# Performance work log

Measured on AMD Instinct MI355X. Metric: run time of the kernel, lower is better.

The kernel has to match this reference:

```python
import jax, jax.numpy as jnp
import numpy as np

B, D, U = 4096, 1024, 1024

def cumax(a):
    # Faithful to source: softmax over last axis, cumsum over axis 0 (TF defaults).
    return jnp.cumsum(jax.nn.softmax(a, axis=-1), axis=0)

def setup_inputs() -> dict:
    key = jax.random.key(0)
    ks = jax.random.split(key, 21)
    names = ['inputs', 'hidden_prev', 'cell_prev',
             'Wf', 'Uf', 'bf', 'Wi', 'Ui', 'bi', 'Wo', 'Uo', 'bo',
             'Wc', 'Uc', 'bc', 'Wft', 'Uft', 'bft', 'Wit', 'Uit', 'bit']
    shapes = [(B, D), (B, U), (B, U)] + [(D, U), (U, U), (U,)] * 6
    scales = [1.0, 1.0, 1.0] + [0.05, 0.05, 0.05] * 6  # random_normal init ~ small stddev
    return {n: jax.random.normal(k, s, dtype=jnp.float32) * sc
            for n, k, s, sc in zip(names, ks, shapes, scales)}

def reference(inputs, hidden_prev, cell_prev,
              Wf, Uf, bf, Wi, Ui, bi, Wo, Uo, bo,
              Wc, Uc, bc, Wft, Uft, bft, Wit, Uit, bit):
    # Fuse the 12 small GEMMs into 2 big ones: [B,D]@[D,6U] and [B,U]@[U,6U]
    W_all = jnp.concatenate([Wf, Wi, Wo, Wc, Wft, Wit], axis=1)   # [D, 6U]
    U_all = jnp.concatenate([Uf, Ui, Uo, Uc, Uft, Uit], axis=1)   # [U, 6U]
    b_all = jnp.concatenate([bf, bi, bo, bc, bft, bit], axis=0)   # [6U]
    pre = inputs @ W_all + hidden_prev @ U_all + b_all            # [B, 6U]
    zf, zi, zo, zc, zft, zit = [pre[:, j*U:(j+1)*U] for j in range(6)]

    f = jax.nn.sigmoid(zf)
    i = jax.nn.sigmoid(zi)
    o = jax.nn.sigmoid(zo)
    c_hat = jnp.tanh(zc)
    f_tilde = cumax(zft)
    i_tilde = 1.0 - cumax(zit)

    omega = f_tilde * i_tilde
    f_hat = f * omega + (f_tilde - omega)
    i_hat = i * omega + (i_tilde - omega)
    cell = f_hat * cell_prev + i_hat * c_hat
    hidden = o * jnp.tanh(cell)
    return hidden, cell
```

## Files before the change

kernel.cpp:

```cpp
#include <hip/hip_runtime.h>
#include <cstdint>
#include <cstddef>


typedef _Float16 half8  __attribute__((ext_vector_type(8)));
typedef _Float16 half4v __attribute__((ext_vector_type(4)));
typedef float f32x4 __attribute__((ext_vector_type(4)));

__device__ __forceinline__ void async16(const _Float16* g, _Float16* l) {
  __builtin_amdgcn_global_load_lds(
      (const __attribute__((address_space(1))) void*)g,
      (__attribute__((address_space(3))) void*)l, 16, 0, 0);
}

struct Ptrs12 { const float* p[12]; };
struct Ptrs6  { const float* p[6];  };

__global__ void prep(const float* __restrict__ X, const float* __restrict__ H,
                     Ptrs12 w, Ptrs6 bs,
                     _Float16* __restrict__ Ahi, _Float16* __restrict__ Bhi,
                     float* __restrict__ b_all) {
  __shared__ float tile[64][65];
  const int blk = blockIdx.x;
  const int t = threadIdx.x;
  if (blk < 8192) {
    size_t base = ((size_t)blk * 256 + t) * 4;
    int k = (int)(base & 2047);
    size_t b = base >> 11;
    const float* src = (k < 1024) ? (X + b * 1024 + k) : (H + b * 1024 + (k - 1024));
    float4 v = *(const float4*)src;
    half4v hi = { (_Float16)v.x, (_Float16)v.y, (_Float16)v.z, (_Float16)v.w };
    *(half4v*)(Ahi + base) = hi;
  } else if (blk < 11264) {
    int bb = blk - 8192;
    int mat = bb >> 8;
    int tl = bb & 255;
    int tr = tl >> 4, tc = tl & 15;
    int g = mat >> 1, s = mat & 1;
    const float* src = w.p[mat];
    int col = t & 63, r0 = t >> 6;
#pragma unroll
    for (int i = 0; i < 16; i++) {
      int row = i * 4 + r0;
      tile[row][col] = src[(size_t)(tr * 64 + row) * 1024 + tc * 64 + col];
    }
    __syncthreads();
    int c2 = t >> 2, kseg = t & 3;
    half8 v0, v1;
#pragma unroll
    for (int j = 0; j < 8; j++) {
      v0[j] = (_Float16)(tile[kseg * 16 + j][c2] * 64.0f);
      v1[j] = (_Float16)(tile[kseg * 16 + 8 + j][c2] * 64.0f);
    }
    size_t n  = (size_t)g * 1024 + tc * 64 + c2;
    size_t kk = (size_t)s * 1024 + tr * 64 + kseg * 16;
    *(half8*)(Bhi + n * 2048 + kk) = v0;
    *(half8*)(Bhi + n * 2048 + kk + 8) = v1;
  } else {
    int n = (blk - 11264) * 256 + t;
    b_all[n] = bs.p[n >> 10][n & 1023];
  }
}


#define LGKM0 asm volatile("s_waitcnt lgkmcnt(0)" ::: "memory")

__device__ __forceinline__ void wg_barrier() {
  __builtin_amdgcn_s_barrier();
  asm volatile("" ::: "memory");
}

__global__ __launch_bounds__(512, 4) void gemm_ring32(
    const _Float16* __restrict__ Ah, const _Float16* __restrict__ Bh,
    const float* __restrict__ b_all, _Float16* __restrict__ pre16) {
  __shared__ __attribute__((aligned(16))) _Float16 lds[36864];

  const int bid = blockIdx.x;
  const int swz = (bid & 7) * 96 + (bid >> 3);
  const int nTile = swz / 32;
  const int mTile = swz % 32;

  const int t = threadIdx.x;
  const int lane = t & 63;
  const int wave = t >> 6;
  const int wm = wave >> 2, wn = wave & 3;
  const int kgrp = lane >> 4, frow = lane & 15;

  const _Float16* Abase = Ah + (size_t)mTile * 128 * 2048;
  const _Float16* Bbase = Bh + (size_t)nTile * 256 * 2048;

  f32x4 acc[4][4] = {};

  auto stage_tile = [&](int kt, int base) {
    {
      int r = t >> 2, sl = t & 3;
      int xs = sl ^ ((r >> 1) & 3);
      async16(Abase + (size_t)r * 2048 + kt * 32 + xs * 8, lds + base + t * 8);
    }
#pragma unroll
    for (int q = 0; q < 2; q++) {
      int s = q * 512 + t;
      int r = s >> 2, sl = s & 3;
      int xs = sl ^ ((r >> 1) & 3);
      async16(Bbase + (size_t)r * 2048 + kt * 32 + xs * 8,
              lds + base + 4096 + s * 8);
    }
  };

  int cur = 0, nxt = 12288, nn = 24576;

  stage_tile(0, cur);
  stage_tile(1, nxt);
  asm volatile("s_waitcnt vmcnt(3)" ::: "memory");
  wg_barrier();

  for (int T = 0; T < 64; T++) {
    const _Float16* A_ = lds + cur;
    const _Float16* B_ = lds + cur + 4096;
    half8 af[4], bf[4];
#pragma unroll
    for (int mi = 0; mi < 4; mi++) {
      int r = wm * 64 + mi * 16 + frow;
      af[mi] = *(const half8*)(A_ + r * 32 + ((kgrp ^ ((r >> 1) & 3)) * 8));
    }
#pragma unroll
    for (int nj = 0; nj < 4; nj++) {
      int r = wn * 64 + nj * 16 + frow;
      bf[nj] = *(const half8*)(B_ + r * 32 + ((kgrp ^ ((r >> 1) & 3)) * 8));
    }
    if (T + 2 < 64) stage_tile(T + 2, nn);

    LGKM0;
    if (T < 62) {
      asm volatile("s_waitcnt vmcnt(3)" ::: "memory");
      wg_barrier();
    } else if (T == 62) {
      asm volatile("s_waitcnt vmcnt(0)" ::: "memory");
      wg_barrier();
    }

    __builtin_amdgcn_s_setprio(1);
#pragma unroll
    for (int mi = 0; mi < 4; mi++)
#pragma unroll
      for (int nj = 0; nj < 4; nj++)
        acc[mi][nj] = __builtin_amdgcn_mfma_f32_16x16x32_f16(
            af[mi], bf[nj], acc[mi][nj], 0, 0, 0);
    __builtin_amdgcn_s_setprio(0);

    int tmp = cur; cur = nxt; nxt = nn; nn = tmp;
  }

  __syncthreads();
  const float inv64 = 1.0f / 64.0f;
  const int cb = nTile * 256;
  float bias[4];
#pragma unroll
  for (int nj = 0; nj < 4; nj++)
    bias[nj] = b_all[cb + wn * 64 + nj * 16 + frow];
#pragma unroll
  for (int mi = 0; mi < 4; mi++) {
#pragma unroll
    for (int nj = 0; nj < 4; nj++) {
      int row = wm * 64 + mi * 16 + kgrp * 4;
      int col = wn * 64 + nj * 16 + frow;
#pragma unroll
      for (int j = 0; j < 4; j++)
        lds[(row + j) * 264 + col] =
            (_Float16)(acc[mi][nj][j] * inv64 + bias[nj]);
    }
  }
  __syncthreads();
#pragma unroll
  for (int rr = 0; rr < 8; rr++) {
    int L = rr * 4096 + t * 8;
    int row = L >> 8, col = L & 255;
    half8 v = *(const half8*)(lds + row * 264 + col);
    *(half8*)(pre16 + (size_t)(mTile * 128 + row) * 6144 + cb + col) = v;
  }
}

__global__ void softmax_partials(_Float16* __restrict__ pre16, f32x4* __restrict__ part4) {
  __shared__ float wsum[4][1024];
  int m = blockIdx.x >> 9;
  int ch = blockIdx.x & 511;
  int t = threadIdx.x;
  int wave = t >> 6, lane = t & 63;
  f32x4 colacc[4] = {};
  for (int rr = 0; rr < 2; rr++) {
    int b = ch * 8 + wave * 2 + rr;
    _Float16* row = pre16 + (size_t)b * 6144 + (4 + m) * 1024;
    f32x4 v[4];
    float mx = -3.4e38f;
#pragma unroll
    for (int j = 0; j < 4; j++) {
      half4v h = *(const half4v*)(row + lane * 4 + 256 * j);
      v[j] = f32x4{ (float)h[0], (float)h[1], (float)h[2], (float)h[3] };
      mx = fmaxf(mx, fmaxf(fmaxf(v[j][0], v[j][1]), fmaxf(v[j][2], v[j][3])));
    }
#pragma unroll
    for (int off = 32; off > 0; off >>= 1) mx = fmaxf(mx, __shfl_xor(mx, off, 64));
    float sum = 0.f;
#pragma unroll
    for (int j = 0; j < 4; j++)
#pragma unroll
      for (int q = 0; q < 4; q++) { v[j][q] = __expf(v[j][q] - mx); sum += v[j][q]; }
#pragma unroll
    for (int off = 32; off > 0; off >>= 1) sum += __shfl_xor(sum, off, 64);
    float inv = 1.f / sum;
#pragma unroll
    for (int j = 0; j < 4; j++) {
      v[j] *= inv;
      half4v h = { (_Float16)v[j][0], (_Float16)v[j][1], (_Float16)v[j][2], (_Float16)v[j][3] };
      *(half4v*)(row + lane * 4 + 256 * j) = h;
      colacc[j] += v[j];
    }
  }
#pragma unroll
  for (int j = 0; j < 4; j++)
    *(f32x4*)(&wsum[wave][lane * 4 + 256 * j]) = colacc[j];
  __syncthreads();
  f32x4 s = *(const f32x4*)(&wsum[0][t * 4]);
  s += *(const f32x4*)(&wsum[1][t * 4]);
  s += *(const f32x4*)(&wsum[2][t * 4]);
  s += *(const f32x4*)(&wsum[3][t * 4]);
  part4[((size_t)m * 256 + t) * 512 + ch] = s;
}

__global__ void scan_partials(const f32x4* __restrict__ part4, f32x4* __restrict__ off4) {
  int gidx = blockIdx.x * 4 + (threadIdx.x >> 6);
  int lane = threadIdx.x & 63;
  size_t base = (size_t)gidx * 512;
  f32x4 v[8];
  f32x4 s = {};
#pragma unroll
  for (int j = 0; j < 8; j++) {
    v[j] = part4[base + lane * 8 + j];
    s += v[j];
  }
  f32x4 incl = s;
#pragma unroll
  for (int off = 1; off < 64; off <<= 1) {
    f32x4 o;
#pragma unroll
    for (int q = 0; q < 4; q++) o[q] = __shfl_up(incl[q], off, 64);
    if (lane >= off) incl += o;
  }
  f32x4 run = incl - s;
#pragma unroll
  for (int j = 0; j < 8; j++) {
    off4[base + lane * 8 + j] = run;
    run += v[j];
  }
}

__device__ __forceinline__ float fast_sigmoid(float x) {
  return __builtin_amdgcn_rcpf(1.f + __expf(-x));
}
__device__ __forceinline__ float fast_tanh(float x) {
  float xc = fminf(fmaxf(x, -15.f), 15.f);
  float e = __expf(2.f * xc);
  return (e - 1.f) * __builtin_amdgcn_rcpf(e + 1.f);
}

__global__ void onlstm_final(const _Float16* __restrict__ pre16,
                             const float* __restrict__ cprev, const f32x4* __restrict__ off4,
                             float* __restrict__ out) {
  int ch = blockIdx.x;
  int c4 = threadIdx.x;
  int c = c4 * 4;
  f32x4 runf = off4[(size_t)c4 * 512 + ch];
  f32x4 runi = off4[(size_t)(256 + c4) * 512 + ch];
  for (int r = 0; r < 8; r++) {
    int b = ch * 8 + r;
    const _Float16* row = pre16 + (size_t)b * 6144;
    half4v zf = *(const half4v*)(row + c);
    half4v zi = *(const half4v*)(row + 1024 + c);
    half4v zo = *(const half4v*)(row + 2048 + c);
    half4v zc = *(const half4v*)(row + 3072 + c);
    half4v pf = *(const half4v*)(row + 4096 + c);
    half4v pi = *(const half4v*)(row + 5120 + c);
    f32x4 cp = *(const f32x4*)(cprev + (size_t)b * 1024 + c);
    f32x4 hid, cel;
#pragma unroll
    for (int q = 0; q < 4; q++) {
      runf[q] += (float)pf[q];
      runi[q] += (float)pi[q];
      float ft = runf[q], it = 1.f - runi[q];
      float f  = fast_sigmoid((float)zf[q]);
      float ii = fast_sigmoid((float)zi[q]);
      float o  = fast_sigmoid((float)zo[q]);
      float chat = fast_tanh((float)zc[q]);
      float omega = ft * it;
      float fhat = f * omega + (ft - omega);
      float ihat = ii * omega + (it - omega);
      float cell = fhat * cp[q] + ihat * chat;
      hid[q] = o * fast_tanh(cell);
      cel[q] = cell;
    }
    *(f32x4*)(out + (size_t)b * 1024 + c) = hid;
    *(f32x4*)(out + (size_t)4194304 + (size_t)b * 1024 + c) = cel;
  }
}

extern "C" void kernel_launch(void* const* d_in, const int* in_sizes, int n_in,
                              void* d_out, int out_size, void* d_ws, size_t ws_size,
                              hipStream_t stream) {
  const float* X = (const float*)d_in[0];
  const float* H = (const float*)d_in[1];
  const float* C = (const float*)d_in[2];

  char* ws = (char*)d_ws;
  _Float16* pre16 = (_Float16*)(ws);
  _Float16* Ahi   = (_Float16*)(ws + 50331648);
  _Float16* Bhi   = (_Float16*)(ws + 67108864);
  float*    b_all = (float*)(ws + 92274688);
  f32x4*    part4 = (f32x4*)(ws + 92299264);
  f32x4*    off4  = (f32x4*)(ws + 96493568);

  Ptrs12 w;
  for (int g = 0; g < 6; g++) {
    w.p[2 * g]     = (const float*)d_in[3 + 3 * g];
    w.p[2 * g + 1] = (const float*)d_in[4 + 3 * g];
  }
  Ptrs6 bs;
  for (int g = 0; g < 6; g++) bs.p[g] = (const float*)d_in[5 + 3 * g];

  prep<<<11288, 256, 0, stream>>>(X, H, w, bs, Ahi, Bhi, b_all);
  gemm_ring32<<<768, 512, 0, stream>>>(Ahi, Bhi, b_all, pre16);
  softmax_partials<<<1024, 256, 0, stream>>>(pre16, part4);
  scan_partials<<<128, 256, 0, stream>>>(part4, off4);
  onlstm_final<<<512, 256, 0, stream>>>(pre16, C, off4, (float*)d_out);
}
```

Baseline: 317.0 us.

## Enlarge GEMM tile to 256x256 and prefetch LDS fragments across MFMA halves

Doubles the GEMM M-tile from 128 to 256 rows, so each workgroup computes a 256x256 output block with 8x4 accumulators per wave, halving the grid to 384 blocks. The K loop is restructured so the next tile's fragments are read from LDS between two halves of the MFMA work, overlapping LDS reads with matrix math. The epilogue writes back in two passes through LDS. This raises arithmetic intensity and cuts global traffic, at the cost of more registers and LDS, lower occupancy (launch bounds 2), and fewer blocks than before to spread across the CUs.

```diff
diff --git a/kernel.cpp b/kernel.cpp
--- a/kernel.cpp
+++ b/kernel.cpp
@@ -70,15 +70,15 @@
   asm volatile("" ::: "memory");
 }
 
-__global__ __launch_bounds__(512, 4) void gemm_ring32(
+__global__ __launch_bounds__(512, 2) void gemm_256(
     const _Float16* __restrict__ Ah, const _Float16* __restrict__ Bh,
     const float* __restrict__ b_all, _Float16* __restrict__ pre16) {
-  __shared__ __attribute__((aligned(16))) _Float16 lds[36864];
+  __shared__ __attribute__((aligned(16))) _Float16 lds[49152];
 
   const int bid = blockIdx.x;
-  const int swz = (bid & 7) * 96 + (bid >> 3);
-  const int nTile = swz / 32;
-  const int mTile = swz % 32;
+  const int swz = (bid & 7) * 48 + (bid >> 3);
+  const int nTile = swz / 16;
+  const int mTile = swz % 16;
 
   const int t = threadIdx.x;
   const int lane = t & 63;
@@ -86,16 +86,18 @@
   const int wm = wave >> 2, wn = wave & 3;
   const int kgrp = lane >> 4, frow = lane & 15;
 
-  const _Float16* Abase = Ah + (size_t)mTile * 128 * 2048;
+  const _Float16* Abase = Ah + (size_t)mTile * 256 * 2048;
   const _Float16* Bbase = Bh + (size_t)nTile * 256 * 2048;
 
-  f32x4 acc[4][4] = {};
+  f32x4 acc[8][4] = {};
 
   auto stage_tile = [&](int kt, int base) {
-    {
-      int r = t >> 2, sl = t & 3;
+#pragma unroll
+    for (int q = 0; q < 2; q++) {
+      int s = q * 512 + t;
+      int r = s >> 2, sl = s & 3;
       int xs = sl ^ ((r >> 1) & 3);
-      async16(Abase + (size_t)r * 2048 + kt * 32 + xs * 8, lds + base + t * 8);
+      async16(Abase + (size_t)r * 2048 + kt * 32 + xs * 8, lds + base + s * 8);
     }
 #pragma unroll
     for (int q = 0; q < 2; q++) {
@@ -103,24 +105,24 @@
       int r = s >> 2, sl = s & 3;
       int xs = sl ^ ((r >> 1) & 3);
       async16(Bbase + (size_t)r * 2048 + kt * 32 + xs * 8,
-              lds + base + 4096 + s * 8);
+              lds + base + 8192 + s * 8);
     }
   };
 
-  int cur = 0, nxt = 12288, nn = 24576;
+  int cur = 0, nxt = 16384, nn = 32768;
 
   stage_tile(0, cur);
   stage_tile(1, nxt);
-  asm volatile("s_waitcnt vmcnt(3)" ::: "memory");
+  asm volatile("s_waitcnt vmcnt(4)" ::: "memory");
   wg_barrier();
 
-  for (int T = 0; T < 64; T++) {
+  half8 af[8], bf[4];
+  {
     const _Float16* A_ = lds + cur;
-    const _Float16* B_ = lds + cur + 4096;
-    half8 af[4], bf[4];
-#pragma unroll
-    for (int mi = 0; mi < 4; mi++) {
-      int r = wm * 64 + mi * 16 + frow;
+    const _Float16* B_ = lds + cur + 8192;
+#pragma unroll
+    for (int mi = 0; mi < 8; mi++) {
+      int r = wm * 128 + mi * 16 + frow;
       af[mi] = *(const half8*)(A_ + r * 32 + ((kgrp ^ ((r >> 1) & 3)) * 8));
     }
 #pragma unroll
@@ -128,26 +130,61 @@
       int r = wn * 64 + nj * 16 + frow;
       bf[nj] = *(const half8*)(B_ + r * 32 + ((kgrp ^ ((r >> 1) & 3)) * 8));
     }
+  }
+
+  for (int T = 0; T < 64; T++) {
+    LGKM0;
     if (T + 2 < 64) stage_tile(T + 2, nn);
 
-    LGKM0;
+    __builtin_amdgcn_s_setprio(1);
+#pragma unroll
+    for (int mi = 0; mi < 4; mi++)
+#pragma unroll
+      for (int nj = 0; nj < 4; nj++)
+        acc[mi][nj] = __builtin_amdgcn_mfma_f32_16x16x32_f16(
+            af[mi], bf[nj], acc[mi][nj], 0, 0, 0);
+    __builtin_amdgcn_s_setprio(0);
+
     if (T < 62) {
-      asm volatile("s_waitcnt vmcnt(3)" ::: "memory");
+      asm volatile("s_waitcnt vmcnt(4)" ::: "memory");
       wg_barrier();
     } else if (T == 62) {
       asm volatile("s_waitcnt vmcnt(0)" ::: "memory");
       wg_barrier();
     }
 
+    const _Float16* An_ = lds + nxt;
+    const _Float16* Bn_ = lds + nxt + 8192;
+    if (T < 63) {
+#pragma unroll
+      for (int mi = 0; mi < 4; mi++) {
+        int r = wm * 128 + mi * 16 + frow;
+        af[mi] = *(const half8*)(An_ + r * 32 + ((kgrp ^ ((r >> 1) & 3)) * 8));
+      }
+    }
+
     __builtin_amdgcn_s_setprio(1);
 #pragma unroll
-    for (int mi = 0; mi < 4; mi++)
+    for (int mi = 4; mi < 8; mi++)
 #pragma unroll
       for (int nj = 0; nj < 4; nj++)
         acc[mi][nj] = __builtin_amdgcn_mfma_f32_16x16x32_f16(
             af[mi], bf[nj], acc[mi][nj], 0, 0, 0);
     __builtin_amdgcn_s_setprio(0);
 
+    if (T < 63) {
+#pragma unroll
+      for (int mi = 4; mi < 8; mi++) {
+        int r = wm * 128 + mi * 16 + frow;
+        af[mi] = *(const half8*)(An_ + r * 32 + ((kgrp ^ ((r >> 1) & 3)) * 8));
+      }
+#pragma unroll
+      for (int nj = 0; nj < 4; nj++) {
+        int r = wn * 64 + nj * 16 + frow;
+        bf[nj] = *(const half8*)(Bn_ + r * 32 + ((kgrp ^ ((r >> 1) & 3)) * 8));
+      }
+    }
+
     int tmp = cur; cur = nxt; nxt = nn; nn = tmp;
   }
 
@@ -158,25 +195,31 @@
 #pragma unroll
   for (int nj = 0; nj < 4; nj++)
     bias[nj] = b_all[cb + wn * 64 + nj * 16 + frow];
-#pragma unroll
-  for (int mi = 0; mi < 4; mi++) {
-#pragma unroll
-    for (int nj = 0; nj < 4; nj++) {
-      int row = wm * 64 + mi * 16 + kgrp * 4;
-      int col = wn * 64 + nj * 16 + frow;
-#pragma unroll
-      for (int j = 0; j < 4; j++)
-        lds[(row + j) * 264 + col] =
-            (_Float16)(acc[mi][nj][j] * inv64 + bias[nj]);
-    }
-  }
-  __syncthreads();
-#pragma unroll
-  for (int rr = 0; rr < 8; rr++) {
-    int L = rr * 4096 + t * 8;
-    int row = L >> 8, col = L & 255;
-    half8 v = *(const half8*)(lds + row * 264 + col);
-    *(half8*)(pre16 + (size_t)(mTile * 128 + row) * 6144 + cb + col) = v;
+
+#pragma unroll
+  for (int pass = 0; pass < 2; pass++) {
+    if (wm == pass) {
+#pragma unroll
+      for (int mi = 0; mi < 8; mi++)
+#pragma unroll
+        for (int nj = 0; nj < 4; nj++) {
+          int row = mi * 16 + kgrp * 4;
+          int col = wn * 64 + nj * 16 + frow;
+#pragma unroll
+          for (int j = 0; j < 4; j++)
+            lds[(row + j) * 264 + col] =
+                (_Float16)(acc[mi][nj][j] * inv64 + bias[nj]);
+        }
+    }
+    __syncthreads();
+#pragma unroll
+    for (int rr = 0; rr < 8; rr++) {
+      int L = rr * 4096 + t * 8;
+      int row = L >> 8, col = L & 255;
+      half8 v = *(const half8*)(lds + row * 264 + col);
+      *(half8*)(pre16 + (size_t)(mTile * 256 + pass * 128 + row) * 6144 + cb + col) = v;
+    }
+    __syncthreads();
   }
 }
 
@@ -327,7 +370,7 @@
   for (int g = 0; g < 6; g++) bs.p[g] = (const float*)d_in[5 + 3 * g];
 
   prep<<<11288, 256, 0, stream>>>(X, H, w, bs, Ahi, Bhi, b_all);
-  gemm_ring32<<<768, 512, 0, stream>>>(Ahi, Bhi, b_all, pre16);
+  gemm_256<<<384, 512, 0, stream>>>(Ahi, Bhi, b_all, pre16);
   softmax_partials<<<1024, 256, 0, stream>>>(pre16, part4);
   scan_partials<<<128, 256, 0, stream>>>(part4, off4);
   onlstm_final<<<512, 256, 0, stream>>>(pre16, C, off4, (float*)d_out);
```

Result: faster. 304.0 us (-4.1%).
